# Kernel tuning notes

Hardware: AMD Instinct MI355X
Metric: run time of the kernel (lower is better)

Reference implementation:

```python
import jax, jax.numpy as jnp
import numpy as np

B = 4096
IN_DIM = 256
OUT_DIM = 256
COND_DIM = 128
HID = 512
HYPER_OUT = IN_DIM * OUT_DIM  # 65536


def setup_inputs() -> dict:
    key = jax.random.key(0)
    ks = jax.random.split(key, 8)

    def xavier(k, shape):
        fan_in, fan_out = shape[0], shape[1]
        std = np.sqrt(2.0 / (fan_in + fan_out))
        return jax.random.normal(k, shape, dtype=jnp.float32) * std

    return {
        "input_h": jax.random.normal(ks[0], (B, IN_DIM), dtype=jnp.float32),
        "condition_z": jax.random.normal(ks[1], (B, COND_DIM), dtype=jnp.float32),
        # hypernet: Linear(COND_DIM, HID) -> ReLU -> Linear(HID, HYPER_OUT)
        "W1": xavier(ks[2], (COND_DIM, HID)),
        "b1": jnp.zeros((HID,), dtype=jnp.float32),
        "W2": xavier(ks[3], (HID, HYPER_OUT)),
        "b2": jnp.zeros((HYPER_OUT,), dtype=jnp.float32),
        # static bias (use_bias=True, generate_bias=False)
        "bias": jnp.zeros((1, OUT_DIM), dtype=jnp.float32),
    }


def reference(input_h, condition_z, W1, b1, W2, b2, bias):
    # HyperNet MLP generates per-sample weight matrix
    hyp = jax.nn.relu(condition_z @ W1 + b1)          # [B, HID]
    weight_S = hyp @ W2 + b2                          # [B, IN*OUT]  (1 GB intermediate)
    weight_S = weight_S.reshape(-1, IN_DIM, OUT_DIM)  # [B, IN, OUT]
    # batched matmul: [B,1,IN] x [B,IN,OUT] -> [B,OUT]
    out = jnp.einsum("bi,bio->bo", input_h, weight_S)
    return out + bias
```

## Files before the change

### kernel.cpp

```cpp
#include <hip/hip_runtime.h>
#include <hip/hip_bf16.h>
#include <stdint.h>


typedef _Float16 f16x8 __attribute__((ext_vector_type(8)));
typedef float    f32x4 __attribute__((ext_vector_type(4)));

#define KTILES     2052
#define TILE_BYTES 32768
#define HB_OFF     (9u*1024u*1024u)
#define BP_OFF     (12u*1024u*1024u)

__global__ void k_init_out(const float* __restrict__ bias, float* __restrict__ out) {
    int idx = blockIdx.x * 256 + threadIdx.x;
    out[idx] = bias[idx & 255];
}

__global__ void k_hcast(const float* __restrict__ h, _Float16* __restrict__ hb) {
    int i = (blockIdx.x * 256 + threadIdx.x) * 8;
    f32x4 a = *(const f32x4*)(h + i);
    f32x4 b = *(const f32x4*)(h + i + 4);
    f16x8 v;
    v[0] = (_Float16)a[0]; v[1] = (_Float16)a[1]; v[2] = (_Float16)a[2]; v[3] = (_Float16)a[3];
    v[4] = (_Float16)b[0]; v[5] = (_Float16)b[1]; v[6] = (_Float16)b[2]; v[7] = (_Float16)b[3];
    *(f16x8*)(hb + i) = v;
}

__global__ void k_hypT(const float* __restrict__ z, const float* __restrict__ W1,
                       const float* __restrict__ b1, float* __restrict__ hypT) {
    int blk = blockIdx.x;
    int t   = threadIdx.x;
    if (blk == 128) {
#pragma unroll
        for (int r = 0; r < 8; ++r) hypT[(size_t)512*4096 + r*512 + t] = 1.0f;
        return;
    }
    __shared__ float zs[32][128];
    int b0 = blk * 32;
#pragma unroll
    for (int u = 0; u < 8; ++u) {
        int idx = u * 512 + t;
        zs[idx >> 7][idx & 127] = z[b0 * 128 + idx];
    }
    __syncthreads();
    float acc[32];
    float bk = b1[t];
#pragma unroll
    for (int b = 0; b < 32; ++b) acc[b] = bk;
    for (int c = 0; c < 128; ++c) {
        float w = W1[c * 512 + t];
#pragma unroll
        for (int b = 0; b < 32; ++b) acc[b] = fmaf(zs[b][c], w, acc[b]);
    }
    float* dst = hypT + (size_t)t * 4096 + b0;
#pragma unroll
    for (int v = 0; v < 8; ++v) {
        f32x4 o;
#pragma unroll
        for (int q = 0; q < 4; ++q) {
            float a = acc[v * 4 + q];
            o[q] = a > 0.f ? a : 0.f;
        }
        *(f32x4*)(dst + v * 4) = o;
    }
}

__global__ void k_pack(const float* __restrict__ W2, const float* __restrict__ b2,
                       _Float16* __restrict__ Bp) {
    __shared__ char tile[TILE_BYTES];
    int t   = blockIdx.x;
    int tid = threadIdx.x;
    long row0 = (long)t * 64;
    const float* src = (t < 2048) ? (W2 + row0 * 256) : (b2 + (row0 - 131072) * 256);
#pragma unroll
    for (int u = 0; u < 16; ++u) {
        int f = (u * 256 + tid) * 4;
        f32x4 v = *(const f32x4*)(src + f);
        int kk = f >> 8;
        int o0 = f & 255;
#pragma unroll
        for (int j = 0; j < 4; ++j) {
            int o = o0 + j;
            int addr = (o * 128 + kk * 2) ^ ((o & 7) << 4);
            *(_Float16*)(tile + addr) = (_Float16)v[j];
        }
    }
    __syncthreads();
    char* dst = (char*)Bp + (size_t)t * TILE_BYTES;
#pragma unroll
    for (int v = 0; v < 8; ++v) {
        int off = (v * 256 + tid) * 16;
        *(f32x4*)(dst + off) = *(const f32x4*)(tile + off);
    }
}

__global__ __launch_bounds__(512, 2) void k_gemm(
        const _Float16* __restrict__ hb, const float* __restrict__ hypT,
        const _Float16* __restrict__ Bp, float* __restrict__ out) {
    __shared__ char smem[131072];

    const int tid  = threadIdx.x;
    const int lane = tid & 63;
    const int wid  = tid >> 6;
    const int wm   = wid >> 2, wn = wid & 3;
    const int l15  = lane & 15, lg = lane >> 4;

    const int bid = blockIdx.x;
    const int s   = bid & 7;
    const int mt  = bid >> 3;
    const int k0  = s * 64;
    const int row_base = mt * 128;
    const int NT  = (s == 7) ? 260 : 256;

    float* shyp = (float*)(smem + 98304);

#pragma unroll
    for (int u = 0; u < 4; ++u) {
        int f  = (u * 512 + tid) * 4;
        int kk = f >> 7;
        int r  = f & 127;
        *(f32x4*)(shyp + kk * 128 + r) =
            *(const f32x4*)(hypT + (size_t)(k0 + kk) * 4096 + row_base + r);
    }

    auto tile_of = [&](int idx) {
        return (idx < 256) ? ((k0 + (idx & 63)) * 4 + (idx >> 6)) : (2048 + idx - 256);
    };
    auto stage = [&](int bufoff, int t) {
        const char* gsrc = (const char*)Bp + (size_t)t * TILE_BYTES + wid * 4096 + lane * 16;
        char* ldst = smem + bufoff + wid * 4096;
#pragma unroll
        for (int q = 0; q < 4; ++q)
            __builtin_amdgcn_global_load_lds(
                (const __attribute__((address_space(1))) void*)(gsrc + q * 1024),
                (__attribute__((address_space(3))) void*)(ldst + q * 1024), 16, 0, 0);
    };

    stage(0,     tile_of(0));
    stage(32768, tile_of(1));
    asm volatile("s_waitcnt vmcnt(4) lgkmcnt(0)" ::: "memory");
    __builtin_amdgcn_s_barrier();

    f32x4 acc[4][4];
#pragma unroll
    for (int i = 0; i < 4; ++i)
#pragma unroll
        for (int j = 0; j < 4; ++j)
#pragma unroll
            for (int q = 0; q < 4; ++q) acc[i][j][q] = 0.0f;

    int boff_read = 0, boff_next = 32768, boff_stage = 65536;

    for (int G = 0; G < 8; ++G) {
        if (G >= 4 && s != 7) break;
        const int niter = (G < 4) ? 64 : 1;

        f16x8 af[4][2];
#pragma unroll
        for (int mf = 0; mf < 4; ++mf)
#pragma unroll
            for (int ks = 0; ks < 2; ++ks)
                af[mf][ks] = *(const f16x8*)(hb + (size_t)(row_base + wm * 64 + mf * 16 + l15) * 256
                                             + (G & 3) * 64 + ks * 32 + lg * 8);

        for (int jj = 0; jj < niter; ++jj) {
            const int idx = (G < 4) ? G * 64 + jj : 256 + (G - 4);
            const bool do_stage = (idx + 2 < NT);
            if (do_stage) stage(boff_stage, tile_of(idx + 2));

            const char* sB = smem + boff_read;
            f16x8 b0[4], b1[4];
#pragma unroll
            for (int nf = 0; nf < 4; ++nf) {
                int col = wn * 64 + nf * 16 + l15;
                int swz = (col & 7) << 4;
                b0[nf] = *(const f16x8*)(sB + ((col * 128 + lg * 16) ^ swz));
                b1[nf] = *(const f16x8*)(sB + ((col * 128 + 64 + lg * 16) ^ swz));
            }
            _Float16 sch[4];
            if (idx < 256) {
#pragma unroll
                for (int mf = 0; mf < 4; ++mf)
                    sch[mf] = (_Float16)shyp[jj * 128 + wm * 64 + mf * 16 + l15];
            } else {
#pragma unroll
                for (int mf = 0; mf < 4; ++mf) sch[mf] = (_Float16)1.0f;
            }

            __builtin_amdgcn_s_setprio(1);
#pragma unroll
            for (int mf = 0; mf < 4; ++mf) {
                f16x8 as0 = af[mf][0] * sch[mf];
                f16x8 as1 = af[mf][1] * sch[mf];
#pragma unroll
                for (int nf = 0; nf < 4; ++nf)
                    acc[mf][nf] = __builtin_amdgcn_mfma_f32_16x16x32_f16(as0, b0[nf], acc[mf][nf], 0, 0, 0);
#pragma unroll
                for (int nf = 0; nf < 4; ++nf)
                    acc[mf][nf] = __builtin_amdgcn_mfma_f32_16x16x32_f16(as1, b1[nf], acc[mf][nf], 0, 0, 0);
            }
            __builtin_amdgcn_s_setprio(0);

            if (do_stage) asm volatile("s_waitcnt vmcnt(4)" ::: "memory");
            else          asm volatile("s_waitcnt vmcnt(0)" ::: "memory");
            __builtin_amdgcn_s_barrier();

            int tmp = boff_read; boff_read = boff_next; boff_next = boff_stage; boff_stage = tmp;
        }
    }

    int crow0 = row_base + wm * 64;
    int ccol0 = wn * 64;
#pragma unroll
    for (int mf = 0; mf < 4; ++mf)
#pragma unroll
        for (int nf = 0; nf < 4; ++nf) {
            int col = ccol0 + nf * 16 + l15;
#pragma unroll
            for (int q = 0; q < 4; ++q) {
                int row = crow0 + mf * 16 + lg * 4 + q;
                atomicAdd(&out[row * 256 + col], acc[mf][nf][q]);
            }
        }
}

extern "C" void kernel_launch(void* const* d_in, const int* in_sizes, int n_in,
                              void* d_out, int out_size, void* d_ws, size_t ws_size,
                              hipStream_t stream) {
    const float* h    = (const float*)d_in[0];
    const float* z    = (const float*)d_in[1];
    const float* W1   = (const float*)d_in[2];
    const float* b1   = (const float*)d_in[3];
    const float* W2   = (const float*)d_in[4];
    const float* b2   = (const float*)d_in[5];
    const float* bias = (const float*)d_in[6];
    float* out = (float*)d_out;

    float*     hypT = (float*)d_ws;
    _Float16*  hb   = (_Float16*)((char*)d_ws + HB_OFF);
    _Float16*  Bp   = (_Float16*)((char*)d_ws + BP_OFF);

    k_pack    <<<KTILES, 256, 0, stream>>>(W2, b2, Bp);
    k_hypT    <<<129,    512, 0, stream>>>(z, W1, b1, hypT);
    k_hcast   <<<512,    256, 0, stream>>>(h, hb);
    k_init_out<<<4096,   256, 0, stream>>>(bias, out);
    k_gemm    <<<256,    512, 0, stream>>>(hb, hypT, Bp, out);
}
```

Measured before the change: 328.2 us.

## Split GEMM output columns across two blocks, halving per-block LDS footprint

The main GEMM now splits the 256 output columns into two halves handled by separate blocks, doubling the grid to 512 blocks. Each block stages only half of each B tile, so the triple-buffered LDS shrinks to 64KB, and the hyper scale is stored in LDS as fp16. Launch bounds rise to 4 blocks per CU to fill the 256 CUs and raise occupancy. The cost is that the A fragments and hyper values are loaded twice, and the extra blocks add atomic adds and per-block work.

```diff
diff --git a/kernel.cpp b/kernel.cpp
--- a/kernel.cpp
+++ b/kernel.cpp
@@ -4,6 +4,7 @@
 
 
 typedef _Float16 f16x8 __attribute__((ext_vector_type(8)));
+typedef _Float16 f16x4 __attribute__((ext_vector_type(4)));
 typedef float    f32x4 __attribute__((ext_vector_type(4)));
 
 #define KTILES     2052
@@ -94,10 +95,10 @@
     }
 }
 
-__global__ __launch_bounds__(512, 2) void k_gemm(
+__global__ __launch_bounds__(512, 4) void k_gemm(
         const _Float16* __restrict__ hb, const float* __restrict__ hypT,
         const _Float16* __restrict__ Bp, float* __restrict__ out) {
-    __shared__ char smem[131072];
+    __shared__ char smem[65536];
 
     const int tid  = threadIdx.x;
     const int lane = tid & 63;
@@ -105,51 +106,57 @@
     const int wm   = wid >> 2, wn = wid & 3;
     const int l15  = lane & 15, lg = lane >> 4;
 
-    const int bid = blockIdx.x;
-    const int s   = bid & 7;
-    const int mt  = bid >> 3;
-    const int k0  = s * 64;
+    const int bid  = blockIdx.x;
+    const int s    = bid & 7;
+    const int rest = bid >> 3;
+    const int nt   = rest & 1;
+    const int mt   = rest >> 1;
+    const int k0   = s * 64;
     const int row_base = mt * 128;
-    const int NT  = (s == 7) ? 260 : 256;
-
-    float* shyp = (float*)(smem + 98304);
+    const int NT   = (s == 7) ? 260 : 256;
+
+    _Float16* shyp = (_Float16*)(smem + 49152);
 
 #pragma unroll
     for (int u = 0; u < 4; ++u) {
         int f  = (u * 512 + tid) * 4;
         int kk = f >> 7;
         int r  = f & 127;
-        *(f32x4*)(shyp + kk * 128 + r) =
-            *(const f32x4*)(hypT + (size_t)(k0 + kk) * 4096 + row_base + r);
+        f32x4 v = *(const f32x4*)(hypT + (size_t)(k0 + kk) * 4096 + row_base + r);
+        f16x4 o;
+        o[0] = (_Float16)v[0]; o[1] = (_Float16)v[1];
+        o[2] = (_Float16)v[2]; o[3] = (_Float16)v[3];
+        *(f16x4*)(shyp + kk * 128 + r) = o;
     }
 
     auto tile_of = [&](int idx) {
         return (idx < 256) ? ((k0 + (idx & 63)) * 4 + (idx >> 6)) : (2048 + idx - 256);
     };
-    auto stage = [&](int bufoff, int t) {
-        const char* gsrc = (const char*)Bp + (size_t)t * TILE_BYTES + wid * 4096 + lane * 16;
-        char* ldst = smem + bufoff + wid * 4096;
-#pragma unroll
-        for (int q = 0; q < 4; ++q)
+    auto stage = [&](int slot, int t) {
+        const char* gsrc = (const char*)Bp + (size_t)t * TILE_BYTES + (nt << 14)
+                         + wid * 2048 + lane * 16;
+        char* ldst = smem + slot * 16384 + wid * 2048;
+#pragma unroll
+        for (int q = 0; q < 2; ++q)
             __builtin_amdgcn_global_load_lds(
                 (const __attribute__((address_space(1))) void*)(gsrc + q * 1024),
                 (__attribute__((address_space(3))) void*)(ldst + q * 1024), 16, 0, 0);
     };
 
-    stage(0,     tile_of(0));
-    stage(32768, tile_of(1));
-    asm volatile("s_waitcnt vmcnt(4) lgkmcnt(0)" ::: "memory");
+    stage(0, tile_of(0));
+    stage(1, tile_of(1));
+    asm volatile("s_waitcnt vmcnt(0) lgkmcnt(0)" ::: "memory");
     __builtin_amdgcn_s_barrier();
 
-    f32x4 acc[4][4];
+    f32x4 acc[4][2];
 #pragma unroll
     for (int i = 0; i < 4; ++i)
 #pragma unroll
-        for (int j = 0; j < 4; ++j)
+        for (int j = 0; j < 2; ++j)
 #pragma unroll
             for (int q = 0; q < 4; ++q) acc[i][j][q] = 0.0f;
 
-    int boff_read = 0, boff_next = 32768, boff_stage = 65536;
+    int slot = 0;
 
     for (int G = 0; G < 8; ++G) {
         if (G >= 4 && s != 7) break;
@@ -166,13 +173,16 @@
         for (int jj = 0; jj < niter; ++jj) {
             const int idx = (G < 4) ? G * 64 + jj : 256 + (G - 4);
             const bool do_stage = (idx + 2 < NT);
-            if (do_stage) stage(boff_stage, tile_of(idx + 2));
-
-            const char* sB = smem + boff_read;
-            f16x8 b0[4], b1[4];
-#pragma unroll
-            for (int nf = 0; nf < 4; ++nf) {
-                int col = wn * 64 + nf * 16 + l15;
+            if (do_stage) {
+                int st = (slot + 2 >= 3) ? slot - 1 : slot + 2;
+                stage(st, tile_of(idx + 2));
+            }
+
+            const char* sB = smem + slot * 16384;
+            f16x8 b0[2], b1[2];
+#pragma unroll
+            for (int nf = 0; nf < 2; ++nf) {
+                int col = wn * 32 + nf * 16 + l15;
                 int swz = (col & 7) << 4;
                 b0[nf] = *(const f16x8*)(sB + ((col * 128 + lg * 16) ^ swz));
                 b1[nf] = *(const f16x8*)(sB + ((col * 128 + 64 + lg * 16) ^ swz));
@@ -181,7 +191,7 @@
             if (idx < 256) {
 #pragma unroll
                 for (int mf = 0; mf < 4; ++mf)
-                    sch[mf] = (_Float16)shyp[jj * 128 + wm * 64 + mf * 16 + l15];
+                    sch[mf] = shyp[jj * 128 + wm * 64 + mf * 16 + l15];
             } else {
 #pragma unroll
                 for (int mf = 0; mf < 4; ++mf) sch[mf] = (_Float16)1.0f;
@@ -193,28 +203,28 @@
                 f16x8 as0 = af[mf][0] * sch[mf];
                 f16x8 as1 = af[mf][1] * sch[mf];
 #pragma unroll
-                for (int nf = 0; nf < 4; ++nf)
+                for (int nf = 0; nf < 2; ++nf)
                     acc[mf][nf] = __builtin_amdgcn_mfma_f32_16x16x32_f16(as0, b0[nf], acc[mf][nf], 0, 0, 0);
 #pragma unroll
-                for (int nf = 0; nf < 4; ++nf)
+                for (int nf = 0; nf < 2; ++nf)
                     acc[mf][nf] = __builtin_amdgcn_mfma_f32_16x16x32_f16(as1, b1[nf], acc[mf][nf], 0, 0, 0);
             }
             __builtin_amdgcn_s_setprio(0);
 
-            if (do_stage) asm volatile("s_waitcnt vmcnt(4)" ::: "memory");
+            if (do_stage) asm volatile("s_waitcnt vmcnt(2)" ::: "memory");
             else          asm volatile("s_waitcnt vmcnt(0)" ::: "memory");
             __builtin_amdgcn_s_barrier();
 
-            int tmp = boff_read; boff_read = boff_next; boff_next = boff_stage; boff_stage = tmp;
+            slot = (slot + 1 >= 3) ? 0 : slot + 1;
         }
     }
 
     int crow0 = row_base + wm * 64;
-    int ccol0 = wn * 64;
+    int ccol0 = nt * 128 + wn * 32;
 #pragma unroll
     for (int mf = 0; mf < 4; ++mf)
 #pragma unroll
-        for (int nf = 0; nf < 4; ++nf) {
+        for (int nf = 0; nf < 2; ++nf) {
             int col = ccol0 + nf * 16 + l15;
 #pragma unroll
             for (int q = 0; q < 4; ++q) {
@@ -244,5 +254,5 @@
     k_hypT    <<<129,    512, 0, stream>>>(z, W1, b1, hypT);
     k_hcast   <<<512,    256, 0, stream>>>(h, hb);
     k_init_out<<<4096,   256, 0, stream>>>(bias, out);
-    k_gemm    <<<256,    512, 0, stream>>>(hb, hypT, Bp, out);
-}
+    k_gemm    <<<512,    512, 0, stream>>>(hb, hypT, Bp, out);
+}
```

Result: slower. 352.2 us (+7.3%).
